# Kernel optimization log

Measured on AMD Instinct MI355X. Metric: run time of the kernel, lower is better.

Reference implementation:

```python
import jax, jax.numpy as jnp
import numpy as np


def setup_inputs() -> dict:
    key = jax.random.key(0)
    ks = jax.random.split(key, 8)
    n, c, h, w = 16, 256, 96, 96
    qk = 4
    x = jax.random.normal(ks[0], (n, c, h, w), dtype=jnp.float32)
    Wq = jax.random.normal(ks[1], (qk, c), dtype=jnp.float32) * 0.05
    Wk = jax.random.normal(ks[2], (qk, c), dtype=jnp.float32) * 0.05
    Wv = jax.random.normal(ks[3], (c, c), dtype=jnp.float32) * 0.05
    W1 = jax.random.normal(ks[4], (c, c), dtype=jnp.float32) * 0.05  # Linear(c, c//ratio), ratio=1
    W2 = jax.random.normal(ks[5], (c, c), dtype=jnp.float32) * 0.05  # Linear(c//ratio, c)
    gama = jax.random.normal(ks[6], (1,), dtype=jnp.float32) * 0.1
    return {"x": x, "Wq": Wq, "Wk": Wk, "Wv": Wv, "W1": W1, "W2": W2, "gama": gama}


def _se_gate(y, W1, W2):
    # SeNet_ChannelAttention: avg & max pool over HxW -> shared MLP -> sigmoid
    avg = jnp.mean(y, axis=(2, 3))            # [n, c]
    mx = jnp.max(y, axis=(2, 3))              # [n, c]
    def mlp(z):
        return jax.nn.relu(z @ W1.T) @ W2.T   # Linear weights are (out, in)
    return jax.nn.sigmoid(mlp(avg) + mlp(mx))  # [n, c]


def reference(x, Wq, Wk, Wv, W1, W2, gama):
    # 1x1 convs as pointwise channel projections
    Q = jnp.einsum('nchw,qc->nqhw', x, Wq)
    K = jnp.einsum('nchw,qc->nqhw', x, Wk)
    V = jnp.einsum('nchw,oc->nohw', x, Wv)

    # Row (width-axis) attention: per (n,h), queries/keys along w
    row_att = jax.nn.softmax(jnp.einsum('nqhw,nqhv->nhwv', Q, K), axis=-1)  # softmax over key pos v
    out1 = jnp.einsum('nchv,nhwv->nchw', V, row_att)

    # Column (height-axis) attention: per (n,w), queries/keys along h
    col_att = jax.nn.softmax(jnp.einsum('nqhw,nqgw->nwhg', Q, K), axis=-1)  # softmax over key pos g
    out2 = jnp.einsum('ncgw,nwhg->nchw', V, col_att)

    out = out1 + out2
    gate = _se_gate(out, W1, W2)              # [n, c]
    out = gate[:, :, None, None] * out
    return gama * out + x
```

## Files before the change

kernel.cpp:

```cpp
#include <hip/hip_runtime.h>
#include <hip/hip_fp16.h>

#define N_  16
#define C_  256
#define H_  96
#define W_  96
#define HW_ 9216
#define QK_ 4

struct alignas(8) h4 { __half2 a, b; };

__device__ inline void h4_unpack(h4 v, float* f) {
    float2 lo = __half22float2(v.a), hi = __half22float2(v.b);
    f[0] = lo.x; f[1] = lo.y; f[2] = hi.x; f[3] = hi.y;
}
__device__ inline h4 h4_pack(float a, float b, float c, float d) {
    h4 r; r.a = __floats2half2_rn(a, b); r.b = __floats2half2_rn(c, d); return r;
}

typedef __attribute__((ext_vector_type(8))) _Float16 f16x8;
typedef __attribute__((ext_vector_type(4))) float    f32x4;


__global__ __launch_bounds__(256) void ccca_rowf(
    const float* __restrict__ x, const float* __restrict__ Wq, const float* __restrict__ Wk,
    float* __restrict__ Qs, float* __restrict__ Ks,
    __half* __restrict__ xTb, __half* __restrict__ Tb)
{
    __shared__ __half XsT[W_][C_ + 4];
    __shared__ __half Ah[W_][100];
    __shared__ float sQ[QK_][W_];
    __shared__ float sK[QK_][W_];
    int t = threadIdx.x;
    int n = blockIdx.x / H_, h = blockIdx.x % H_;
    const float* xb = x + (size_t)n * C_ * HW_ + (size_t)h * W_;
    for (int i = t; i < C_ * (W_ / 4); i += 256) {
        int c = i / 24, s4 = (i % 24) * 4;
        float4 v = *(const float4*)(xb + (size_t)c * HW_ + s4);
        XsT[s4    ][c] = __float2half(v.x);
        XsT[s4 + 1][c] = __float2half(v.y);
        XsT[s4 + 2][c] = __float2half(v.z);
        XsT[s4 + 3][c] = __float2half(v.w);
    }
    __syncthreads();
    {
        __half* xd = xTb + ((size_t)n * W_ * H_ + h) * C_;
        for (int i = t; i < W_ * (C_ / 4); i += 256) {
            int w = i / 64, s = (i % 64) * 4;
            *(h4*)(xd + (size_t)w * H_ * C_ + s) = *(const h4*)&XsT[w][s];
        }
    }
    for (int i = t; i < 2 * QK_ * W_; i += 256) {
        int sel = i / (QK_ * W_), r = i % (QK_ * W_);
        int q = r / W_, w = r % W_;
        const float* wr = (sel ? Wk : Wq) + q * C_;
        float s = 0.f;
        for (int c = 0; c < C_; ++c) s = fmaf(wr[c], __half2float(XsT[w][c]), s);
        if (sel) { sK[q][w] = s; Ks[(((size_t)n * QK_ + q) * H_ + h) * W_ + w] = s; }
        else     { sQ[q][w] = s; Qs[(((size_t)n * QK_ + q) * H_ + h) * W_ + w] = s; }
    }
    __syncthreads();
    for (int i = t; i < W_ * W_; i += 256) {
        int w = i / W_, v = i % W_;
        float s = 0.f;
        #pragma unroll
        for (int q = 0; q < QK_; ++q) s = fmaf(sQ[q][w], sK[q][v], s);
        Ah[w][v] = __float2half(s);
    }
    __syncthreads();
    if (t < W_) {
        float m = -1e30f;
        for (int v = 0; v < W_; ++v) m = fmaxf(m, __half2float(Ah[t][v]));
        float sum = 0.f;
        for (int v = 0; v < W_; ++v) {
            float e = __expf(__half2float(Ah[t][v]) - m);
            sum += e;
            Ah[t][v] = __float2half(e);
        }
        float inv = 1.f / sum;
        for (int v = 0; v < W_; ++v)
            Ah[t][v] = __float2half(__half2float(Ah[t][v]) * inv);
    }
    __syncthreads();
    int to = t >> 4, tw = t & 15;
    __half* Tn = Tb + ((size_t)n * H_ + h) * W_ * C_;
    for (int ot = 0; ot < 4; ++ot) {
        int ob = ot * 64 + to * 4;
        float acc[4][6];
        #pragma unroll
        for (int i = 0; i < 4; ++i)
            #pragma unroll
            for (int j = 0; j < 6; ++j) acc[i][j] = 0.f;
        for (int v = 0; v < W_; ++v) {
            float xr[4];
            h4_unpack(*(const h4*)&XsT[v][ob], xr);
            float ar[6];
            #pragma unroll
            for (int j = 0; j < 6; ++j) ar[j] = __half2float(Ah[tw * 6 + j][v]);
            #pragma unroll
            for (int i = 0; i < 4; ++i)
                #pragma unroll
                for (int j = 0; j < 6; ++j) acc[i][j] = fmaf(xr[i], ar[j], acc[i][j]);
        }
        #pragma unroll
        for (int j = 0; j < 6; ++j) {
            int w = tw * 6 + j;
            *(h4*)(Tn + (size_t)w * C_ + ob) =
                h4_pack(acc[0][j], acc[1][j], acc[2][j], acc[3][j]);
        }
    }
}

__global__ __launch_bounds__(256) void ccca_col2(
    const float* __restrict__ Qs, const float* __restrict__ Ks,
    const __half* __restrict__ xTb, __half* __restrict__ Tb)
{
    __shared__ __half XTw[H_][C_ + 4];
    __shared__ __half Ah[H_][100];
    __shared__ float sQ[QK_][H_];
    __shared__ float sK[QK_][H_];
    int t = threadIdx.x;
    int n = blockIdx.x / W_, w = blockIdx.x % W_;
    for (int i = t; i < 2 * QK_ * H_; i += 256) {
        int sel = i / (QK_ * H_), r = i % (QK_ * H_);
        int q = r / H_, g = r % H_;
        float v = (sel ? Ks : Qs)[(((size_t)n * QK_ + q) * H_ + g) * W_ + w];
        if (sel) sK[q][g] = v; else sQ[q][g] = v;
    }
    const __half* src = xTb + ((size_t)n * W_ + w) * H_ * C_;
    for (int i = t; i < H_ * (C_ / 4); i += 256) {
        int g = i / 64, s = (i % 64) * 4;
        *(h4*)&XTw[g][s] = *(const h4*)(src + (size_t)g * C_ + s);
    }
    __syncthreads();
    for (int i = t; i < H_ * H_; i += 256) {
        int hh = i / H_, g = i % H_;
        float s = 0.f;
        #pragma unroll
        for (int q = 0; q < QK_; ++q) s = fmaf(sQ[q][hh], sK[q][g], s);
        Ah[hh][g] = __float2half(s);
    }
    __syncthreads();
    if (t < H_) {
        float m = -1e30f;
        for (int g = 0; g < H_; ++g) m = fmaxf(m, __half2float(Ah[t][g]));
        float sum = 0.f;
        for (int g = 0; g < H_; ++g) {
            float e = __expf(__half2float(Ah[t][g]) - m);
            sum += e;
            Ah[t][g] = __float2half(e);
        }
        float inv = 1.f / sum;
        for (int g = 0; g < H_; ++g)
            Ah[t][g] = __float2half(__half2float(Ah[t][g]) * inv);
    }
    __syncthreads();
    int to = t >> 4, th = t & 15;
    for (int ot = 0; ot < 4; ++ot) {
        int ob = ot * 64 + to * 4;
        float acc[4][6];
        #pragma unroll
        for (int i = 0; i < 4; ++i)
            #pragma unroll
            for (int j = 0; j < 6; ++j) acc[i][j] = 0.f;
        for (int g = 0; g < H_; ++g) {
            float xr[4];
            h4_unpack(*(const h4*)&XTw[g][ob], xr);
            float ar[6];
            #pragma unroll
            for (int j = 0; j < 6; ++j) ar[j] = __half2float(Ah[th * 6 + j][g]);
            #pragma unroll
            for (int i = 0; i < 4; ++i)
                #pragma unroll
                for (int j = 0; j < 6; ++j) acc[i][j] = fmaf(xr[i], ar[j], acc[i][j]);
        }
        #pragma unroll
        for (int j = 0; j < 6; ++j) {
            int hh = th * 6 + j;
            __half* p = Tb + (((size_t)n * H_ + hh) * W_ + w) * C_ + ob;
            float old[4];
            h4_unpack(*(const h4*)p, old);
            *(h4*)p = h4_pack(old[0] + acc[0][j], old[1] + acc[1][j],
                              old[2] + acc[2][j], old[3] + acc[3][j]);
        }
    }
}

__global__ __launch_bounds__(256) void ccca_cvtwv(
    const float* __restrict__ Wv, __half* __restrict__ Wvh)
{
    int gid = blockIdx.x * 256 + threadIdx.x;
    float4 v = ((const float4*)Wv)[gid];
    ((h4*)Wvh)[gid] = h4_pack(v.x, v.y, v.z, v.w);
}

__global__ __launch_bounds__(256) void ccca_wvm(
    const __half* __restrict__ Tb, const __half* __restrict__ Wvh,
    __half* __restrict__ OPb, float* __restrict__ psum, float* __restrict__ pmax)
{
    int t = threadIdx.x;
    int wd = t >> 6, lane = t & 63;
    int ln15 = lane & 15, kg = lane >> 4;
    int n = blockIdx.x / 144, tile = blockIdx.x % 144;

    const _Float16* Ab = (const _Float16*)Wvh + (size_t)(64 * wd + ln15) * C_ + kg * 8;
    const _Float16* Bb = (const _Float16*)Tb +
                         ((size_t)n * HW_ + tile * 64 + ln15) * C_ + kg * 8;

    f32x4 acc[4][4];
    #pragma unroll
    for (int i = 0; i < 4; ++i)
        #pragma unroll
        for (int p = 0; p < 4; ++p) acc[i][p] = (f32x4){0.f, 0.f, 0.f, 0.f};

    #pragma unroll
    for (int kk = 0; kk < 8; ++kk) {
        f16x8 a[4], b[4];
        #pragma unroll
        for (int i = 0; i < 4; ++i)
            a[i] = *(const f16x8*)(Ab + (size_t)i * 16 * C_ + kk * 32);
        #pragma unroll
        for (int p = 0; p < 4; ++p)
            b[p] = *(const f16x8*)(Bb + (size_t)p * 16 * C_ + kk * 32);
        #pragma unroll
        for (int i = 0; i < 4; ++i)
            #pragma unroll
            for (int p = 0; p < 4; ++p)
                acc[i][p] = __builtin_amdgcn_mfma_f32_16x16x32_f16(a[i], b[p], acc[i][p], 0, 0, 0);
    }

    __half* dst = OPb + (size_t)n * C_ * HW_;
    #pragma unroll
    for (int i = 0; i < 4; ++i) {
        #pragma unroll
        for (int r = 0; r < 4; ++r) {
            int c = 64 * wd + 16 * i + 4 * kg + r;
            #pragma unroll
            for (int p = 0; p < 4; ++p) {
                int px = tile * 64 + 16 * p + ln15;
                dst[(size_t)c * HW_ + px] = __float2half(acc[i][p][r]);
            }
        }
    }

    #pragma unroll
    for (int i = 0; i < 4; ++i) {
        float ps[4] = {0.f, 0.f, 0.f, 0.f};
        float pm[4] = {-1e30f, -1e30f, -1e30f, -1e30f};
        #pragma unroll
        for (int p = 0; p < 4; ++p)
            #pragma unroll
            for (int r = 0; r < 4; ++r) {
                ps[r] += acc[i][p][r];
                pm[r] = fmaxf(pm[r], acc[i][p][r]);
            }
        #pragma unroll
        for (int m = 1; m <= 8; m <<= 1)
            #pragma unroll
            for (int r = 0; r < 4; ++r) {
                ps[r] += __shfl_xor(ps[r], m);
                pm[r] = fmaxf(pm[r], __shfl_xor(pm[r], m));
            }
        if (ln15 == 0) {
            size_t base = ((size_t)n * 144 + tile) * C_ + 64 * wd + 16 * i + 4 * kg;
            #pragma unroll
            for (int r = 0; r < 4; ++r) { psum[base + r] = ps[r]; pmax[base + r] = pm[r]; }
        }
    }
}

__global__ __launch_bounds__(256) void ccca_wv1(
    const __half* __restrict__ Tb, const float* __restrict__ Wv,
    __half* __restrict__ OPb, float* __restrict__ psum, float* __restrict__ pmax)
{
    __shared__ __half Ts[64][C_ + 4];
    __shared__ float sWv[C_][36];
    int t = threadIdx.x;
    int n = blockIdx.x / 144, tile = blockIdx.x % 144;
    const __half* src = Tb + ((size_t)n * HW_ + tile * 64) * C_;
    for (int i = t; i < 64 * 64; i += 256) {
        int px = i / 64, s = (i % 64) * 4;
        *(h4*)&Ts[px][s] = *(const h4*)(src + (size_t)px * C_ + s);
    }
    int cb = t >> 4, pb = t & 15;
    float acc[16][4];
    #pragma unroll
    for (int j = 0; j < 16; ++j)
        #pragma unroll
        for (int p = 0; p < 4; ++p) acc[j][p] = 0.f;
    for (int ob = 0; ob < 8; ++ob) {
        __syncthreads();
        for (int i = t; i < C_ * 8; i += 256) {
            int r = i / 8, s = (i % 8) * 4;
            *(float4*)&sWv[r][s] = *(const float4*)(Wv + (size_t)r * C_ + ob * 32 + s);
        }
        __syncthreads();
        for (int oc = 0; oc < 32; oc += 4) {
            float tv[4][4];
            #pragma unroll
            for (int p = 0; p < 4; ++p)
                h4_unpack(*(const h4*)&Ts[pb * 4 + p][ob * 32 + oc], tv[p]);
            #pragma unroll
            for (int j = 0; j < 16; ++j) {
                float4 wv4 = *(const float4*)&sWv[cb * 16 + j][oc];
                #pragma unroll
                for (int p = 0; p < 4; ++p) {
                    acc[j][p] = fmaf(wv4.x, tv[p][0], acc[j][p]);
                    acc[j][p] = fmaf(wv4.y, tv[p][1], acc[j][p]);
                    acc[j][p] = fmaf(wv4.z, tv[p][2], acc[j][p]);
                    acc[j][p] = fmaf(wv4.w, tv[p][3], acc[j][p]);
                }
            }
        }
    }
    __half* dst = OPb + (size_t)n * C_ * HW_ + tile * 64;
    #pragma unroll
    for (int j = 0; j < 16; ++j) {
        int c = cb * 16 + j;
        *(h4*)(dst + (size_t)c * HW_ + pb * 4) =
            h4_pack(acc[j][0], acc[j][1], acc[j][2], acc[j][3]);
    }
    #pragma unroll
    for (int j = 0; j < 16; ++j) {
        float s = acc[j][0] + acc[j][1] + acc[j][2] + acc[j][3];
        float m = fmaxf(fmaxf(acc[j][0], acc[j][1]), fmaxf(acc[j][2], acc[j][3]));
        #pragma unroll
        for (int off = 1; off <= 8; off <<= 1) {
            s += __shfl_xor(s, off);
            m = fmaxf(m, __shfl_xor(m, off));
        }
        if (pb == 0) {
            size_t o = ((size_t)n * 144 + tile) * C_ + cb * 16 + j;
            psum[o] = s;
            pmax[o] = m;
        }
    }
}

__global__ __launch_bounds__(256) void ccca_gate2(
    const float* __restrict__ psum, const float* __restrict__ pmax,
    const float* __restrict__ W1, const float* __restrict__ W2,
    float* __restrict__ gate)
{
    __shared__ float sa[C_], sm[C_], hs[C_];
    int n = blockIdx.x, t = threadIdx.x;
    float s = 0.f, m = -1e30f;
    for (int i = 0; i < 144; ++i) {
        s += psum[((size_t)n * 144 + i) * C_ + t];
        m = fmaxf(m, pmax[((size_t)n * 144 + i) * C_ + t]);
    }
    sa[t] = s * (1.f / 9216.f);
    sm[t] = m;
    __syncthreads();
    const float* w1r = W1 + (size_t)t * C_;
    float aa = 0.f, am = 0.f;
    for (int i = 0; i < C_; ++i) { float wv = w1r[i]; aa = fmaf(wv, sa[i], aa); am = fmaf(wv, sm[i], am); }
    hs[t] = fmaxf(aa, 0.f) + fmaxf(am, 0.f);
    __syncthreads();
    const float* w2r = W2 + (size_t)t * C_;
    float g = 0.f;
    for (int i = 0; i < C_; ++i) g = fmaf(w2r[i], hs[i], g);
    gate[n * C_ + t] = 1.f / (1.f + __expf(-g));
}

__global__ __launch_bounds__(256) void ccca_final2(
    const float* __restrict__ x, const __half* __restrict__ OPb,
    const float* __restrict__ gate, const float* __restrict__ gama,
    float* __restrict__ out)
{
    float g0 = gama[0];
    const size_t total = (size_t)N_ * C_ * HW_ / 4;
    for (size_t i = (size_t)blockIdx.x * 256 + threadIdx.x; i < total; i += (size_t)gridDim.x * 256) {
        float4 xv = ((const float4*)x)[i];
        float ov[4];
        h4_unpack(((const h4*)OPb)[i], ov);
        size_t nc = (i * 4) / HW_;
        float sc = g0 * gate[nc];
        float4 r;
        r.x = fmaf(sc, ov[0], xv.x);
        r.y = fmaf(sc, ov[1], xv.y);
        r.z = fmaf(sc, ov[2], xv.z);
        r.w = fmaf(sc, ov[3], xv.w);
        ((float4*)out)[i] = r;
    }
}


__global__ __launch_bounds__(256) void ccca_qk(
    const float* __restrict__ x, const float* __restrict__ Wq,
    const float* __restrict__ Wk, float* __restrict__ Qo, float* __restrict__ Ko)
{
    __shared__ float sWq[QK_ * C_];
    __shared__ float sWk[QK_ * C_];
    int t = threadIdx.x;
    for (int i = t; i < QK_ * C_; i += 256) { sWq[i] = Wq[i]; sWk[i] = Wk[i]; }
    __syncthreads();
    int n = blockIdx.x / 36;
    int p = (blockIdx.x % 36) * 256 + t;
    const float* xp = x + (size_t)n * C_ * HW_ + p;
    float qa[QK_] = {0.f, 0.f, 0.f, 0.f};
    float ka[QK_] = {0.f, 0.f, 0.f, 0.f};
    for (int c = 0; c < C_; ++c) {
        float v = xp[(size_t)c * HW_];
        #pragma unroll
        for (int q = 0; q < QK_; ++q) {
            qa[q] = fmaf(v, sWq[q * C_ + c], qa[q]);
            ka[q] = fmaf(v, sWk[q * C_ + c], ka[q]);
        }
    }
    size_t base = (size_t)n * QK_ * HW_ + p;
    #pragma unroll
    for (int q = 0; q < QK_; ++q) { Qo[base + q * HW_] = qa[q]; Ko[base + q * HW_] = ka[q]; }
}

__global__ __launch_bounds__(256) void ccca_row(
    const float* __restrict__ x, const float* __restrict__ Qw,
    const float* __restrict__ Kw, float* __restrict__ out)
{
    __shared__ float sQ[QK_][W_];
    __shared__ float sK[QK_][W_];
    __shared__ float A[W_][W_ + 1];
    __shared__ float Xs[64][W_ + 1];
    int t = threadIdx.x;
    int n = blockIdx.x / H_;
    int h = blockIdx.x % H_;
    for (int i = t; i < QK_ * W_; i += 256) {
        int q = i / W_, w = i % W_;
        size_t off = ((size_t)n * QK_ + q) * HW_ + h * W_ + w;
        sQ[q][w] = Qw[off];
        sK[q][w] = Kw[off];
    }
    __syncthreads();
    for (int i = t; i < W_ * W_; i += 256) {
        int w = i / W_, v = i % W_;
        float s = 0.f;
        #pragma unroll
        for (int q = 0; q < QK_; ++q) s = fmaf(sQ[q][w], sK[q][v], s);
        A[w][v] = s;
    }
    __syncthreads();
    if (t < W_) {
        float m = -1e30f;
        for (int v = 0; v < W_; ++v) m = fmaxf(m, A[t][v]);
        float sum = 0.f;
        for (int v = 0; v < W_; ++v) { float e = __expf(A[t][v] - m); A[t][v] = e; sum += e; }
        float inv = 1.f / sum;
        for (int v = 0; v < W_; ++v) A[t][v] *= inv;
    }
    __syncthreads();
    int to = t >> 4, tw = t & 15;
    for (int ot = 0; ot < 4; ++ot) {
        for (int i = t; i < 64 * W_ / 4; i += 256) {
            int f = i * 4;
            int o = f / W_, v = f % W_;
            float4 val = *(const float4*)(x + (((size_t)n * C_ + ot * 64 + o) * H_ + h) * W_ + v);
            Xs[o][v] = val.x; Xs[o][v + 1] = val.y; Xs[o][v + 2] = val.z; Xs[o][v + 3] = val.w;
        }
        __syncthreads();
        float acc[4][6];
        #pragma unroll
        for (int i = 0; i < 4; ++i)
            #pragma unroll
            for (int j = 0; j < 6; ++j) acc[i][j] = 0.f;
        for (int v = 0; v < W_; ++v) {
            float xr[4], ar[6];
            #pragma unroll
            for (int i = 0; i < 4; ++i) xr[i] = Xs[to * 4 + i][v];
            #pragma unroll
            for (int j = 0; j < 6; ++j) ar[j] = A[tw * 6 + j][v];
            #pragma unroll
            for (int i = 0; i < 4; ++i)
                #pragma unroll
                for (int j = 0; j < 6; ++j) acc[i][j] = fmaf(xr[i], ar[j], acc[i][j]);
        }
        #pragma unroll
        for (int i = 0; i < 4; ++i) {
            size_t ob = (((size_t)n * C_ + ot * 64 + to * 4 + i) * H_ + h) * W_ + tw * 6;
            #pragma unroll
            for (int j = 0; j < 6; ++j) out[ob + j] = acc[i][j];
        }
        __syncthreads();
    }
}

__global__ __launch_bounds__(256) void ccca_col(
    const float* __restrict__ x, const float* __restrict__ Qw,
    const float* __restrict__ Kw, float* __restrict__ out)
{
    __shared__ float sQ[QK_][H_];
    __shared__ float sK[QK_][H_];
    __shared__ float A[H_][H_ + 1];
    __shared__ float Xc[64][H_ + 1];
    int t = threadIdx.x;
    int n = blockIdx.x / W_;
    int w = blockIdx.x % W_;
    for (int i = t; i < QK_ * H_; i += 256) {
        int q = i / H_, hh = i % H_;
        size_t off = ((size_t)n * QK_ + q) * HW_ + hh * W_ + w;
        sQ[q][hh] = Qw[off];
        sK[q][hh] = Kw[off];
    }
    __syncthreads();
    for (int i = t; i < H_ * H_; i += 256) {
        int hh = i / H_, g = i % H_;
        float s = 0.f;
        #pragma unroll
        for (int q = 0; q < QK_; ++q) s = fmaf(sQ[q][hh], sK[q][g], s);
        A[hh][g] = s;
    }
    __syncthreads();
    if (t < H_) {
        float m = -1e30f;
        for (int g = 0; g < H_; ++g) m = fmaxf(m, A[t][g]);
        float sum = 0.f;
        for (int g = 0; g < H_; ++g) { float e = __expf(A[t][g] - m); A[t][g] = e; sum += e; }
        float inv = 1.f / sum;
        for (int g = 0; g < H_; ++g) A[t][g] *= inv;
    }
    __syncthreads();
    int to = t >> 4, th = t & 15;
    for (int ot = 0; ot < 4; ++ot) {
        for (int i = t; i < 64 * H_; i += 256) {
            int o = i / H_, g = i % H_;
            Xc[o][g] = x[(((size_t)n * C_ + ot * 64 + o) * H_ + g) * W_ + w];
        }
        __syncthreads();
        float acc[4][6];
        #pragma unroll
        for (int i = 0; i < 4; ++i)
            #pragma unroll
            for (int j = 0; j < 6; ++j) acc[i][j] = 0.f;
        for (int g = 0; g < H_; ++g) {
            float xr[4], ar[6];
            #pragma unroll
            for (int i = 0; i < 4; ++i) xr[i] = Xc[to * 4 + i][g];
            #pragma unroll
            for (int j = 0; j < 6; ++j) ar[j] = A[th * 6 + j][g];
            #pragma unroll
            for (int i = 0; i < 4; ++i)
                #pragma unroll
                for (int j = 0; j < 6; ++j) acc[i][j] = fmaf(xr[i], ar[j], acc[i][j]);
        }
        #pragma unroll
        for (int i = 0; i < 4; ++i)
            #pragma unroll
            for (int j = 0; j < 6; ++j) {
                size_t ob = (((size_t)n * C_ + ot * 64 + to * 4 + i) * H_ + th * 6 + j) * W_ + w;
                out[ob] += acc[i][j];
            }
        __syncthreads();
    }
}

__global__ __launch_bounds__(256) void ccca_wv(
    const float* __restrict__ Wv, float* __restrict__ out)
{
    __shared__ float Ts[C_][64];
    int t = threadIdx.x;
    int n = blockIdx.x / 144;
    int p0 = (blockIdx.x % 144) * 64;
    float* base = out + (size_t)n * C_ * HW_ + p0;
    for (int i = t; i < C_ * 16; i += 256) {
        int o = i >> 4, p4 = (i & 15) << 2;
        *(float4*)&Ts[o][p4] = *(const float4*)(base + (size_t)o * HW_ + p4);
    }
    __syncthreads();
    int cb = t >> 4, pb = t & 15;
    float acc[16][4];
    #pragma unroll
    for (int j = 0; j < 16; ++j)
        #pragma unroll
        for (int p = 0; p < 4; ++p) acc[j][p] = 0.f;
    for (int o = 0; o < C_; o += 4) {
        float tvv[4][4];
        #pragma unroll
        for (int k = 0; k < 4; ++k) {
            float4 q = *(float4*)&Ts[o + k][pb * 4];
            tvv[k][0] = q.x; tvv[k][1] = q.y; tvv[k][2] = q.z; tvv[k][3] = q.w;
        }
        #pragma unroll
        for (int j = 0; j < 16; ++j) {
            float4 wv = *(const float4*)(Wv + (size_t)(cb * 16 + j) * C_ + o);
            float wvv[4] = {wv.x, wv.y, wv.z, wv.w};
            #pragma unroll
            for (int k = 0; k < 4; ++k)
                #pragma unroll
                for (int p = 0; p < 4; ++p)
                    acc[j][p] = fmaf(wvv[k], tvv[k][p], acc[j][p]);
        }
    }
    #pragma unroll
    for (int j = 0; j < 16; ++j) {
        float4 r; r.x = acc[j][0]; r.y = acc[j][1]; r.z = acc[j][2]; r.w = acc[j][3];
        *(float4*)(base + (size_t)(cb * 16 + j) * HW_ + pb * 4) = r;
    }
}

__global__ __launch_bounds__(256) void ccca_pool(
    const float* __restrict__ out, float* __restrict__ avg, float* __restrict__ mx)
{
    int nc = blockIdx.x;
    const float* p = out + (size_t)nc * HW_;
    int t = threadIdx.x;
    float s = 0.f, m = -1e30f;
    for (int i = t; i < HW_; i += 256) { float v = p[i]; s += v; m = fmaxf(m, v); }
    #pragma unroll
    for (int off = 32; off > 0; off >>= 1) {
        s += __shfl_down(s, off);
        m = fmaxf(m, __shfl_down(m, off));
    }
    __shared__ float ss[4], smx[4];
    int wv = t >> 6;
    if ((t & 63) == 0) { ss[wv] = s; smx[wv] = m; }
    __syncthreads();
    if (t == 0) {
        s = ss[0] + ss[1] + ss[2] + ss[3];
        m = fmaxf(fmaxf(smx[0], smx[1]), fmaxf(smx[2], smx[3]));
        avg[nc] = s * (1.f / 9216.f);
        mx[nc] = m;
    }
}

__global__ __launch_bounds__(256) void ccca_gate(
    const float* __restrict__ avg, const float* __restrict__ mx,
    const float* __restrict__ W1, const float* __restrict__ W2,
    float* __restrict__ gate)
{
    __shared__ float sa[C_], sm[C_], hs[C_];
    int n = blockIdx.x, t = threadIdx.x;
    sa[t] = avg[n * C_ + t];
    sm[t] = mx[n * C_ + t];
    __syncthreads();
    const float* w1r = W1 + (size_t)t * C_;
    float aa = 0.f, am = 0.f;
    for (int i = 0; i < C_; ++i) { float wv = w1r[i]; aa = fmaf(wv, sa[i], aa); am = fmaf(wv, sm[i], am); }
    hs[t] = fmaxf(aa, 0.f) + fmaxf(am, 0.f);
    __syncthreads();
    const float* w2r = W2 + (size_t)t * C_;
    float g = 0.f;
    for (int i = 0; i < C_; ++i) g = fmaf(w2r[i], hs[i], g);
    gate[n * C_ + t] = 1.f / (1.f + __expf(-g));
}

__global__ __launch_bounds__(256) void ccca_final(
    const float* __restrict__ x, const float* __restrict__ gate,
    const float* __restrict__ gama, float* __restrict__ out)
{
    float g0 = gama[0];
    const size_t total = (size_t)N_ * C_ * HW_ / 4;
    for (size_t i = (size_t)blockIdx.x * 256 + threadIdx.x; i < total; i += (size_t)gridDim.x * 256) {
        float4 o = ((const float4*)out)[i];
        float4 xv = ((const float4*)x)[i];
        size_t nc = (i * 4) / HW_;
        float sc = g0 * gate[nc];
        o.x = fmaf(sc, o.x, xv.x);
        o.y = fmaf(sc, o.y, xv.y);
        o.z = fmaf(sc, o.z, xv.z);
        o.w = fmaf(sc, o.w, xv.w);
        ((float4*)out)[i] = o;
    }
}


extern "C" void kernel_launch(void* const* d_in, const int* in_sizes, int n_in,
                              void* d_out, int out_size, void* d_ws, size_t ws_size,
                              hipStream_t stream)
{
    const float* x    = (const float*)d_in[0];
    const float* Wq   = (const float*)d_in[1];
    const float* Wk   = (const float*)d_in[2];
    const float* Wv   = (const float*)d_in[3];
    const float* W1   = (const float*)d_in[4];
    const float* W2   = (const float*)d_in[5];
    const float* gama = (const float*)d_in[6];
    float* out = (float*)d_out;
    char*  ws  = (char*)d_ws;

    const size_t TBE      = (size_t)N_ * HW_ * C_;
    const size_t WS_NEED  = 155729920ull;
    const size_t WS_NEED2 = WS_NEED + 131072ull;

    if (ws_size >= WS_NEED) {
        __half* xTb  = (__half*)ws;
        __half* Tb   = (__half*)(ws + TBE * 2);
        float*  Qs   = (float*)(ws + TBE * 4);
        float*  Ks   = Qs + (size_t)N_ * QK_ * HW_;
        float*  gate = (float*)(ws + TBE * 4 + 4718592);
        __half* Wvh  = (__half*)(ws + WS_NEED);
        ccca_rowf<<<N_ * H_, 256, 0, stream>>>(x, Wq, Wk, Qs, Ks, xTb, Tb);
        ccca_col2<<<N_ * W_, 256, 0, stream>>>(Qs, Ks, xTb, Tb);
        if (ws_size >= WS_NEED2) {
            ccca_cvtwv<<<64, 256, 0, stream>>>(Wv, Wvh);
            ccca_wvm<<<N_ * 144, 256, 0, stream>>>(Tb, Wvh, xTb, Qs, Ks);
        } else {
            ccca_wv1<<<N_ * 144, 256, 0, stream>>>(Tb, Wv, xTb, Qs, Ks);
        }
        ccca_gate2<<<N_, 256, 0, stream>>>(Qs, Ks, W1, W2, gate);
        ccca_final2<<<2048, 256, 0, stream>>>(x, xTb, gate, gama, out);
    } else {
        float* wsf = (float*)ws;
        const size_t QSZ = (size_t)N_ * QK_ * HW_;
        float* Qb   = wsf;
        float* Kb   = wsf + QSZ;
        float* avg  = wsf + 2 * QSZ;
        float* mx   = avg + N_ * C_;
        float* gate = mx + N_ * C_;
        ccca_qk  <<<N_ * 36, 256, 0, stream>>>(x, Wq, Wk, Qb, Kb);
        ccca_row <<<N_ * H_, 256, 0, stream>>>(x, Qb, Kb, out);
        ccca_col <<<N_ * W_, 256, 0, stream>>>(x, Qb, Kb, out);
        ccca_wv  <<<N_ * 144, 256, 0, stream>>>(Wv, out);
        ccca_pool<<<N_ * C_, 256, 0, stream>>>(out, avg, mx);
        ccca_gate<<<N_, 256, 0, stream>>>(avg, mx, W1, W2, gate);
        ccca_final<<<2048, 256, 0, stream>>>(x, gate, gama, out);
    }
}
```

Baseline: 760.6 us.

## Move row/column attention aggregation to MFMA with separate Q/K projection kernel

Splits the Q/K projection into its own kernel, which also writes x in a column-blocked fp16 layout for the column pass. The row and column attention-times-V-input products now use MFMA 16x16x32 f16 instructions instead of scalar FMA loops. The fallback scalar Wv path is removed, and workspace buffers are aliased. The column kernel's read-modify-write of Tb now uses scattered scalar half accesses, which may cost memory efficiency.

```diff
diff --git a/kernel.cpp b/kernel.cpp
--- a/kernel.cpp
+++ b/kernel.cpp
@@ -22,42 +22,70 @@
 typedef __attribute__((ext_vector_type(4))) float    f32x4;
 
 
-__global__ __launch_bounds__(256) void ccca_rowf(
+__global__ __launch_bounds__(192) void ccca_qkt(
     const float* __restrict__ x, const float* __restrict__ Wq, const float* __restrict__ Wk,
-    float* __restrict__ Qs, float* __restrict__ Ks,
-    __half* __restrict__ xTb, __half* __restrict__ Tb)
-{
-    __shared__ __half XsT[W_][C_ + 4];
-    __shared__ __half Ah[W_][100];
-    __shared__ float sQ[QK_][W_];
-    __shared__ float sK[QK_][W_];
+    __half* __restrict__ xP, float* __restrict__ Qs, float* __restrict__ Ks)
+{
+    __shared__ float sW[8][C_];
+    int t = threadIdx.x;
+    int n = blockIdx.x / 12, gt = blockIdx.x % 12;
+    for (int i = t; i < 8 * C_; i += 192)
+        sW[i / C_][i % C_] = (i < 4 * C_) ? Wq[i] : Wk[i - 4 * C_];
+    __syncthreads();
+    int w = t % 96, gsub = t / 96;
+    float accQ[4][4], accK[4][4];
+    #pragma unroll
+    for (int k = 0; k < 4; ++k)
+        #pragma unroll
+        for (int q = 0; q < 4; ++q) { accQ[k][q] = 0.f; accK[k][q] = 0.f; }
+    const float* xb = x + (size_t)n * C_ * HW_ + (size_t)(gt * 8 + gsub * 4) * W_ + w;
+    __half* xpd = xP + (((size_t)n * 12 + gt) * W_ + w) * 2048 + gsub * 4;
+    for (int c = 0; c < C_; ++c) {
+        float xv[4];
+        #pragma unroll
+        for (int k = 0; k < 4; ++k) xv[k] = xb[(size_t)c * HW_ + k * W_];
+        *(h4*)(xpd + (size_t)c * 8) = h4_pack(xv[0], xv[1], xv[2], xv[3]);
+        #pragma unroll
+        for (int q = 0; q < QK_; ++q) {
+            float wq = sW[q][c], wk = sW[4 + q][c];
+            #pragma unroll
+            for (int k = 0; k < 4; ++k) {
+                accQ[k][q] = fmaf(wq, xv[k], accQ[k][q]);
+                accK[k][q] = fmaf(wk, xv[k], accK[k][q]);
+            }
+        }
+    }
+    #pragma unroll
+    for (int k = 0; k < 4; ++k) {
+        int g = gt * 8 + gsub * 4 + k;
+        #pragma unroll
+        for (int q = 0; q < QK_; ++q) {
+            Qs[(((size_t)n * QK_ + q) * H_ + g) * W_ + w] = accQ[k][q];
+            Ks[(((size_t)n * QK_ + q) * H_ + g) * W_ + w] = accK[k][q];
+        }
+    }
+}
+
+__global__ __launch_bounds__(256) void ccca_rowm(
+    const float* __restrict__ x, const float* __restrict__ Qs, const float* __restrict__ Ks,
+    __half* __restrict__ Tb)
+{
+    __shared__ __half Xs[C_][104];
+    __shared__ __half A1[W_][104];
+    __shared__ float sQ[QK_][W_], sK[QK_][W_];
     int t = threadIdx.x;
     int n = blockIdx.x / H_, h = blockIdx.x % H_;
     const float* xb = x + (size_t)n * C_ * HW_ + (size_t)h * W_;
-    for (int i = t; i < C_ * (W_ / 4); i += 256) {
-        int c = i / 24, s4 = (i % 24) * 4;
-        float4 v = *(const float4*)(xb + (size_t)c * HW_ + s4);
-        XsT[s4    ][c] = __float2half(v.x);
-        XsT[s4 + 1][c] = __float2half(v.y);
-        XsT[s4 + 2][c] = __float2half(v.z);
-        XsT[s4 + 3][c] = __float2half(v.w);
-    }
-    __syncthreads();
-    {
-        __half* xd = xTb + ((size_t)n * W_ * H_ + h) * C_;
-        for (int i = t; i < W_ * (C_ / 4); i += 256) {
-            int w = i / 64, s = (i % 64) * 4;
-            *(h4*)(xd + (size_t)w * H_ * C_ + s) = *(const h4*)&XsT[w][s];
-        }
+    for (int i = t; i < C_ * 24; i += 256) {
+        int c = i / 24, v4 = (i % 24) * 4;
+        float4 v = *(const float4*)(xb + (size_t)c * HW_ + v4);
+        *(h4*)&Xs[c][v4] = h4_pack(v.x, v.y, v.z, v.w);
     }
     for (int i = t; i < 2 * QK_ * W_; i += 256) {
         int sel = i / (QK_ * W_), r = i % (QK_ * W_);
         int q = r / W_, w = r % W_;
-        const float* wr = (sel ? Wk : Wq) + q * C_;
-        float s = 0.f;
-        for (int c = 0; c < C_; ++c) s = fmaf(wr[c], __half2float(XsT[w][c]), s);
-        if (sel) { sK[q][w] = s; Ks[(((size_t)n * QK_ + q) * H_ + h) * W_ + w] = s; }
-        else     { sQ[q][w] = s; Qs[(((size_t)n * QK_ + q) * H_ + h) * W_ + w] = s; }
+        float v = (sel ? Ks : Qs)[(((size_t)n * QK_ + q) * H_ + h) * W_ + w];
+        if (sel) sK[q][w] = v; else sQ[q][w] = v;
     }
     __syncthreads();
     for (int i = t; i < W_ * W_; i += 256) {
@@ -65,125 +93,132 @@
         float s = 0.f;
         #pragma unroll
         for (int q = 0; q < QK_; ++q) s = fmaf(sQ[q][w], sK[q][v], s);
-        Ah[w][v] = __float2half(s);
+        A1[w][v] = __float2half(s);
     }
     __syncthreads();
     if (t < W_) {
         float m = -1e30f;
-        for (int v = 0; v < W_; ++v) m = fmaxf(m, __half2float(Ah[t][v]));
+        for (int v = 0; v < W_; ++v) m = fmaxf(m, __half2float(A1[t][v]));
         float sum = 0.f;
         for (int v = 0; v < W_; ++v) {
-            float e = __expf(__half2float(Ah[t][v]) - m);
-            sum += e;
-            Ah[t][v] = __float2half(e);
+            float e = __expf(__half2float(A1[t][v]) - m);
+            sum += e; A1[t][v] = __float2half(e);
         }
         float inv = 1.f / sum;
         for (int v = 0; v < W_; ++v)
-            Ah[t][v] = __float2half(__half2float(Ah[t][v]) * inv);
-    }
-    __syncthreads();
-    int to = t >> 4, tw = t & 15;
+            A1[t][v] = __float2half(__half2float(A1[t][v]) * inv);
+    }
+    __syncthreads();
+    int wd = t >> 6, lane = t & 63, ln15 = lane & 15, kg = lane >> 4;
+    f32x4 acc[4][6];
+    #pragma unroll
+    for (int i = 0; i < 4; ++i)
+        #pragma unroll
+        for (int p = 0; p < 6; ++p) acc[i][p] = (f32x4){0.f, 0.f, 0.f, 0.f};
+    #pragma unroll
+    for (int kk = 0; kk < 3; ++kk) {
+        f16x8 a[4], b[6];
+        #pragma unroll
+        for (int i = 0; i < 4; ++i)
+            a[i] = *(const f16x8*)&Xs[64 * wd + 16 * i + ln15][kk * 32 + kg * 8];
+        #pragma unroll
+        for (int p = 0; p < 6; ++p)
+            b[p] = *(const f16x8*)&A1[16 * p + ln15][kk * 32 + kg * 8];
+        #pragma unroll
+        for (int i = 0; i < 4; ++i)
+            #pragma unroll
+            for (int p = 0; p < 6; ++p)
+                acc[i][p] = __builtin_amdgcn_mfma_f32_16x16x32_f16(a[i], b[p], acc[i][p], 0, 0, 0);
+    }
     __half* Tn = Tb + ((size_t)n * H_ + h) * W_ * C_;
-    for (int ot = 0; ot < 4; ++ot) {
-        int ob = ot * 64 + to * 4;
-        float acc[4][6];
-        #pragma unroll
-        for (int i = 0; i < 4; ++i)
-            #pragma unroll
-            for (int j = 0; j < 6; ++j) acc[i][j] = 0.f;
-        for (int v = 0; v < W_; ++v) {
-            float xr[4];
-            h4_unpack(*(const h4*)&XsT[v][ob], xr);
-            float ar[6];
-            #pragma unroll
-            for (int j = 0; j < 6; ++j) ar[j] = __half2float(Ah[tw * 6 + j][v]);
-            #pragma unroll
-            for (int i = 0; i < 4; ++i)
-                #pragma unroll
-                for (int j = 0; j < 6; ++j) acc[i][j] = fmaf(xr[i], ar[j], acc[i][j]);
-        }
-        #pragma unroll
-        for (int j = 0; j < 6; ++j) {
-            int w = tw * 6 + j;
-            *(h4*)(Tn + (size_t)w * C_ + ob) =
-                h4_pack(acc[0][j], acc[1][j], acc[2][j], acc[3][j]);
-        }
-    }
-}
-
-__global__ __launch_bounds__(256) void ccca_col2(
-    const float* __restrict__ Qs, const float* __restrict__ Ks,
-    const __half* __restrict__ xTb, __half* __restrict__ Tb)
-{
-    __shared__ __half XTw[H_][C_ + 4];
-    __shared__ __half Ah[H_][100];
-    __shared__ float sQ[QK_][H_];
-    __shared__ float sK[QK_][H_];
+    #pragma unroll
+    for (int i = 0; i < 4; ++i) {
+        int c0 = 64 * wd + 16 * i + 4 * kg;
+        #pragma unroll
+        for (int p = 0; p < 6; ++p) {
+            int w = 16 * p + ln15;
+            *(h4*)(Tn + (size_t)w * C_ + c0) =
+                h4_pack(acc[i][p][0], acc[i][p][1], acc[i][p][2], acc[i][p][3]);
+        }
+    }
+}
+
+__global__ __launch_bounds__(256) void ccca_colm(
+    const __half* __restrict__ xP, const float* __restrict__ Qs, const float* __restrict__ Ks,
+    __half* __restrict__ Tb)
+{
+    __shared__ __half Xs[C_][104];
+    __shared__ __half A2[H_][104];
+    __shared__ float sQ[QK_][H_], sK[QK_][H_];
     int t = threadIdx.x;
     int n = blockIdx.x / W_, w = blockIdx.x % W_;
+    for (int i = t; i < 12 * C_; i += 256) {
+        int gb = i >> 8, c = i & 255;
+        f16x8 v = *(const f16x8*)(xP + (((size_t)n * 12 + gb) * W_ + w) * 2048 + (size_t)c * 8);
+        *(f16x8*)&Xs[c][gb * 8] = v;
+    }
     for (int i = t; i < 2 * QK_ * H_; i += 256) {
         int sel = i / (QK_ * H_), r = i % (QK_ * H_);
         int q = r / H_, g = r % H_;
         float v = (sel ? Ks : Qs)[(((size_t)n * QK_ + q) * H_ + g) * W_ + w];
         if (sel) sK[q][g] = v; else sQ[q][g] = v;
     }
-    const __half* src = xTb + ((size_t)n * W_ + w) * H_ * C_;
-    for (int i = t; i < H_ * (C_ / 4); i += 256) {
-        int g = i / 64, s = (i % 64) * 4;
-        *(h4*)&XTw[g][s] = *(const h4*)(src + (size_t)g * C_ + s);
-    }
     __syncthreads();
     for (int i = t; i < H_ * H_; i += 256) {
         int hh = i / H_, g = i % H_;
         float s = 0.f;
         #pragma unroll
         for (int q = 0; q < QK_; ++q) s = fmaf(sQ[q][hh], sK[q][g], s);
-        Ah[hh][g] = __float2half(s);
+        A2[hh][g] = __float2half(s);
     }
     __syncthreads();
     if (t < H_) {
         float m = -1e30f;
-        for (int g = 0; g < H_; ++g) m = fmaxf(m, __half2float(Ah[t][g]));
+        for (int g = 0; g < H_; ++g) m = fmaxf(m, __half2float(A2[t][g]));
         float sum = 0.f;
         for (int g = 0; g < H_; ++g) {
-            float e = __expf(__half2float(Ah[t][g]) - m);
-            sum += e;
-            Ah[t][g] = __float2half(e);
+            float e = __expf(__half2float(A2[t][g]) - m);
+            sum += e; A2[t][g] = __float2half(e);
         }
         float inv = 1.f / sum;
         for (int g = 0; g < H_; ++g)
-            Ah[t][g] = __float2half(__half2float(Ah[t][g]) * inv);
-    }
-    __syncthreads();
-    int to = t >> 4, th = t & 15;
-    for (int ot = 0; ot < 4; ++ot) {
-        int ob = ot * 64 + to * 4;
-        float acc[4][6];
-        #pragma unroll
-        for (int i = 0; i < 4; ++i)
-            #pragma unroll
-            for (int j = 0; j < 6; ++j) acc[i][j] = 0.f;
-        for (int g = 0; g < H_; ++g) {
-            float xr[4];
-            h4_unpack(*(const h4*)&XTw[g][ob], xr);
-            float ar[6];
-            #pragma unroll
-            for (int j = 0; j < 6; ++j) ar[j] = __half2float(Ah[th * 6 + j][g]);
-            #pragma unroll
-            for (int i = 0; i < 4; ++i)
-                #pragma unroll
-                for (int j = 0; j < 6; ++j) acc[i][j] = fmaf(xr[i], ar[j], acc[i][j]);
-        }
-        #pragma unroll
-        for (int j = 0; j < 6; ++j) {
-            int hh = th * 6 + j;
-            __half* p = Tb + (((size_t)n * H_ + hh) * W_ + w) * C_ + ob;
-            float old[4];
-            h4_unpack(*(const h4*)p, old);
-            *(h4*)p = h4_pack(old[0] + acc[0][j], old[1] + acc[1][j],
-                              old[2] + acc[2][j], old[3] + acc[3][j]);
-        }
-    }
+            A2[t][g] = __float2half(__half2float(A2[t][g]) * inv);
+    }
+    __syncthreads();
+    int wd = t >> 6, lane = t & 63, ln15 = lane & 15, kg = lane >> 4;
+    f32x4 acc[6][4];
+    #pragma unroll
+    for (int i = 0; i < 6; ++i)
+        #pragma unroll
+        for (int p = 0; p < 4; ++p) acc[i][p] = (f32x4){0.f, 0.f, 0.f, 0.f};
+    #pragma unroll
+    for (int kk = 0; kk < 3; ++kk) {
+        f16x8 a[6], b[4];
+        #pragma unroll
+        for (int i = 0; i < 6; ++i)
+            a[i] = *(const f16x8*)&A2[16 * i + ln15][kk * 32 + kg * 8];
+        #pragma unroll
+        for (int p = 0; p < 4; ++p)
+            b[p] = *(const f16x8*)&Xs[64 * wd + 16 * p + ln15][kk * 32 + kg * 8];
+        #pragma unroll
+        for (int i = 0; i < 6; ++i)
+            #pragma unroll
+            for (int p = 0; p < 4; ++p)
+                acc[i][p] = __builtin_amdgcn_mfma_f32_16x16x32_f16(a[i], b[p], acc[i][p], 0, 0, 0);
+    }
+    __half* Tn = Tb + (size_t)n * HW_ * C_;
+    #pragma unroll
+    for (int i = 0; i < 6; ++i)
+        #pragma unroll
+        for (int p = 0; p < 4; ++p) {
+            int c = 64 * wd + 16 * p + ln15;
+            #pragma unroll
+            for (int r = 0; r < 4; ++r) {
+                int hh = 16 * i + 4 * kg + r;
+                __half* ptr = Tn + ((size_t)hh * W_ + w) * C_ + c;
+                *ptr = __float2half(__half2float(*ptr) + acc[i][p][r]);
+            }
+        }
 }
 
 __global__ __launch_bounds__(256) void ccca_cvtwv(
@@ -265,74 +300,6 @@
             size_t base = ((size_t)n * 144 + tile) * C_ + 64 * wd + 16 * i + 4 * kg;
             #pragma unroll
             for (int r = 0; r < 4; ++r) { psum[base + r] = ps[r]; pmax[base + r] = pm[r]; }
-        }
-    }
-}
-
-__global__ __launch_bounds__(256) void ccca_wv1(
-    const __half* __restrict__ Tb, const float* __restrict__ Wv,
-    __half* __restrict__ OPb, float* __restrict__ psum, float* __restrict__ pmax)
-{
-    __shared__ __half Ts[64][C_ + 4];
-    __shared__ float sWv[C_][36];
-    int t = threadIdx.x;
-    int n = blockIdx.x / 144, tile = blockIdx.x % 144;
-    const __half* src = Tb + ((size_t)n * HW_ + tile * 64) * C_;
-    for (int i = t; i < 64 * 64; i += 256) {
-        int px = i / 64, s = (i % 64) * 4;
-        *(h4*)&Ts[px][s] = *(const h4*)(src + (size_t)px * C_ + s);
-    }
-    int cb = t >> 4, pb = t & 15;
-    float acc[16][4];
-    #pragma unroll
-    for (int j = 0; j < 16; ++j)
-        #pragma unroll
-        for (int p = 0; p < 4; ++p) acc[j][p] = 0.f;
-    for (int ob = 0; ob < 8; ++ob) {
-        __syncthreads();
-        for (int i = t; i < C_ * 8; i += 256) {
-            int r = i / 8, s = (i % 8) * 4;
-            *(float4*)&sWv[r][s] = *(const float4*)(Wv + (size_t)r * C_ + ob * 32 + s);
-        }
-        __syncthreads();
-        for (int oc = 0; oc < 32; oc += 4) {
-            float tv[4][4];
-            #pragma unroll
-            for (int p = 0; p < 4; ++p)
-                h4_unpack(*(const h4*)&Ts[pb * 4 + p][ob * 32 + oc], tv[p]);
-            #pragma unroll
-            for (int j = 0; j < 16; ++j) {
-                float4 wv4 = *(const float4*)&sWv[cb * 16 + j][oc];
-                #pragma unroll
-                for (int p = 0; p < 4; ++p) {
-                    acc[j][p] = fmaf(wv4.x, tv[p][0], acc[j][p]);
-                    acc[j][p] = fmaf(wv4.y, tv[p][1], acc[j][p]);
-                    acc[j][p] = fmaf(wv4.z, tv[p][2], acc[j][p]);
-                    acc[j][p] = fmaf(wv4.w, tv[p][3], acc[j][p]);
-                }
-            }
-        }
-    }
-    __half* dst = OPb + (size_t)n * C_ * HW_ + tile * 64;
-    #pragma unroll
-    for (int j = 0; j < 16; ++j) {
-        int c = cb * 16 + j;
-        *(h4*)(dst + (size_t)c * HW_ + pb * 4) =
-            h4_pack(acc[j][0], acc[j][1], acc[j][2], acc[j][3]);
-    }
-    #pragma unroll
-    for (int j = 0; j < 16; ++j) {
-        float s = acc[j][0] + acc[j][1] + acc[j][2] + acc[j][3];
-        float m = fmaxf(fmaxf(acc[j][0], acc[j][1]), fmaxf(acc[j][2], acc[j][3]));
-        #pragma unroll
-        for (int off = 1; off <= 8; off <<= 1) {
-            s += __shfl_xor(s, off);
-            m = fmaxf(m, __shfl_xor(m, off));
-        }
-        if (pb == 0) {
-            size_t o = ((size_t)n * 144 + tile) * C_ + cb * 16 + j;
-            psum[o] = s;
-            pmax[o] = m;
         }
     }
 }
@@ -676,27 +643,26 @@
     float* out = (float*)d_out;
     char*  ws  = (char*)d_ws;
 
-    const size_t TBE      = (size_t)N_ * HW_ * C_;
-    const size_t WS_NEED  = 155729920ull;
-    const size_t WS_NEED2 = WS_NEED + 131072ull;
-
-    if (ws_size >= WS_NEED) {
-        __half* xTb  = (__half*)ws;
-        __half* Tb   = (__half*)(ws + TBE * 2);
-        float*  Qs   = (float*)(ws + TBE * 4);
-        float*  Ks   = Qs + (size_t)N_ * QK_ * HW_;
-        float*  gate = (float*)(ws + TBE * 4 + 4718592);
-        __half* Wvh  = (__half*)(ws + WS_NEED);
-        ccca_rowf<<<N_ * H_, 256, 0, stream>>>(x, Wq, Wk, Qs, Ks, xTb, Tb);
-        ccca_col2<<<N_ * W_, 256, 0, stream>>>(Qs, Ks, xTb, Tb);
-        if (ws_size >= WS_NEED2) {
-            ccca_cvtwv<<<64, 256, 0, stream>>>(Wv, Wvh);
-            ccca_wvm<<<N_ * 144, 256, 0, stream>>>(Tb, Wvh, xTb, Qs, Ks);
-        } else {
-            ccca_wv1<<<N_ * 144, 256, 0, stream>>>(Tb, Wv, xTb, Qs, Ks);
-        }
-        ccca_gate2<<<N_, 256, 0, stream>>>(Qs, Ks, W1, W2, gate);
-        ccca_final2<<<2048, 256, 0, stream>>>(x, xTb, gate, gama, out);
+    const size_t WS_NEED3 = 155844608ull;
+
+    if (ws_size >= WS_NEED3) {
+        __half* xP   = (__half*)ws;
+        __half* Tb   = (__half*)(ws + 75497472ull);
+        float*  Qs   = (float*)(ws + 150994944ull);
+        float*  Ks   = (float*)(ws + 153354240ull);
+        __half* Wvh  = (__half*)(ws + 155713536ull);
+        float*  psum = Qs;
+        float*  pmax = Ks;
+        float*  gate = (float*)Tb;
+        __half* OPb  = xP;
+
+        ccca_qkt  <<<N_ * 12, 192, 0, stream>>>(x, Wq, Wk, xP, Qs, Ks);
+        ccca_cvtwv<<<64, 256, 0, stream>>>(Wv, Wvh);
+        ccca_rowm <<<N_ * H_, 256, 0, stream>>>(x, Qs, Ks, Tb);
+        ccca_colm <<<N_ * W_, 256, 0, stream>>>(xP, Qs, Ks, Tb);
+        ccca_wvm  <<<N_ * 144, 256, 0, stream>>>(Tb, Wvh, OPb, psum, pmax);
+        ccca_gate2<<<N_, 256, 0, stream>>>(psum, pmax, W1, W2, gate);
+        ccca_final2<<<2048, 256, 0, stream>>>(x, OPb, gate, gama, out);
     } else {
         float* wsf = (float*)ws;
         const size_t QSZ = (size_t)N_ * QK_ * HW_;
```

Result: faster. 701.8 us (-7.7%).
